# Performance work log

Hardware: AMD Instinct MI355X
Metric: run time of the kernel (lower is better)

Reference implementation:

```python
import jax, jax.numpy as jnp
import numpy as np

jax.config.update("jax_enable_x64", True)

P = 2038074743          # prime used by the ROBE-Z hash
BLOCK_K = 32            # tile sizes of the hashed reconstruction (kernel tile)
BLOCK_N = 32
INPUT_DIM = 8192
OUTPUT_DIM = 8192
HASH_SIZE = 1 << 22     # compressed parameter count
TOKENS = 512


def setup_inputs() -> dict:
    key = jax.random.key(0)
    k1, k2 = jax.random.split(key, 2)
    x = jax.random.normal(k1, (TOKENS, INPUT_DIM), dtype=jnp.float32)
    hashed_weight = jax.random.normal(k2, (HASH_SIZE,), dtype=jnp.float32) * 0.02
    bias = jnp.zeros((OUTPUT_DIM,), dtype=jnp.float32)
    # mirrors RzLinear._generate_random_numbers(seed): 4 random ints made even, prepended with P
    rng = np.random.RandomState(1024)
    r = rng.randint(0, P, size=(4,)).astype(np.int64)
    r = r + (r % 2)
    random_numbers = jnp.asarray(np.concatenate([np.array([P], dtype=np.int64), r]), dtype=jnp.int64)
    return {"x": x, "hashed_weight": hashed_weight, "bias": bias, "random_numbers": random_numbers}


def _weight_indices(random_numbers):
    """Hashed flat indices into hashed_weight for the dense [K, N] weight."""
    K, N = INPUT_DIM, OUTPUT_DIM
    kt, nt = K // BLOCK_K, N // BLOCK_N
    R1, R2, R3 = random_numbers[1], random_numbers[2], random_numbers[3]
    k_ids = jnp.arange(kt, dtype=jnp.int64)
    n_ids = jnp.arange(nt, dtype=jnp.int64)
    # per-tile start offset into the compressed array
    start = ((k_ids[:, None] * R3 + n_ids[None, :] * R2 + R1) % P) % (HASH_SIZE - BLOCK_K * BLOCK_N + 1)
    start = start.astype(jnp.int32)  # [kt, nt]
    off = (jnp.arange(BLOCK_K, dtype=jnp.int32)[:, None] * BLOCK_N
           + jnp.arange(BLOCK_N, dtype=jnp.int32)[None, :])  # [BK, BN], row-major within tile
    idx = start[:, None, :, None] + off[None, :, None, :]    # [kt, BK, nt, BN]
    return idx.reshape(K, N)


def reference(x, hashed_weight, bias, random_numbers):
    idx = _weight_indices(random_numbers)          # [K, N] int32
    W = hashed_weight[idx]                          # hashed-gather reconstruction, [K, N]
    out = jnp.matmul(x, W) + bias[None, :]          # [tokens, N]
    return out
```

## Files before the change

### kernel.cpp

```cpp
#include <hip/hip_runtime.h>
#include <hip/hip_fp16.h>

#define NDIM 8192
#define KDIM 8192
#define NT 256
#define MOD2 4193281
#define PRIME 2038074743LL

#define BM 128
#define BN 128
#define BK 32
#define KITER 64
#define ASTRIDE 40
#define BSLAB 1032

typedef _Float16 half8 __attribute__((ext_vector_type(8)));
typedef float floatx4 __attribute__((ext_vector_type(4)));

#define BARRIER() asm volatile("s_waitcnt lgkmcnt(0)\n\ts_barrier" ::: "memory")

__global__ __launch_bounds__(256) void prep_kernel(const float* __restrict__ x,
                                                   const float* __restrict__ hw,
                                                   const float* __restrict__ bias,
                                                   const int* __restrict__ rn,
                                                   __half* __restrict__ xh,
                                                   __half* __restrict__ hh,
                                                   int* __restrict__ starts,
                                                   float* __restrict__ out) {
    int b = blockIdx.x;
    int tid = threadIdx.x;
    if (b < 8192) {
        int i = b * 256 + tid;
        const float4* s; uint2* d; int j;
        if (i < (1 << 20)) { s = (const float4*)x;  d = (uint2*)xh; j = i; }
        else               { s = (const float4*)hw; d = (uint2*)hh; j = i - (1 << 20); }
        float4 v = s[j];
        __half2 h01 = __floats2half2_rn(v.x, v.y);
        __half2 h23 = __floats2half2_rn(v.z, v.w);
        uint2 w = {*(unsigned*)&h01, *(unsigned*)&h23};
        d[j] = w;
    } else if (b < 8192 + 4096) {
        int i = (b - 8192) * 256 + tid;
        float4 bv = *(const float4*)(bias + ((i & 2047) << 2));
        ((float4*)out)[i] = bv;
    } else {
        int t = (b - 12288) * 256 + tid;
        bool is64 = (rn[1] == 0 && rn[3] == 0);
        long long R1 = is64 ? rn[2] : rn[1];
        long long R2 = is64 ? rn[4] : rn[2];
        long long R3 = is64 ? rn[6] : rn[3];
        long long k_id = t >> 8, n_id = t & 255;
        long long v = (k_id * R3 + n_id * R2 + R1) % PRIME;
        starts[t] = (int)(v % MOD2);
    }
}

__global__ __launch_bounds__(256, 4) void gemm_kernel(
    const __half* __restrict__ xh, const __half* __restrict__ hh,
    const int* __restrict__ starts, float* __restrict__ out) {
    __shared__ __align__(16) __half As[2][BM * ASTRIDE];
    __shared__ __align__(16) __half Bs[2][4 * BSLAB];
    __shared__ int Ss[KITER * 4];

    const int tid = threadIdx.x;
    const int lane = tid & 63;
    const int wave = tid >> 6;
    const int wm = wave >> 1;
    const int wn = wave & 1;
    const int quad = lane >> 4;
    const int l16 = lane & 15;

    const int i = blockIdx.x;
    const int ks = i & 3;
    const int m_blk = (i >> 2) & 3;
    const int n_blk = i >> 4;
    const int gm0 = m_blk * BM;
    const int gn0 = n_blk * BN;
    const int kt0 = ks * KITER;
    const int n_id0 = n_blk * 4;

    Ss[tid] = starts[(kt0 + (tid >> 2)) * NT + n_id0 + (tid & 3)];

    const int a_row = tid >> 1;
    const int a_ch = tid & 1;
    const __half* aptr = xh + (size_t)(gm0 + a_row) * KDIM + kt0 * 32 + a_ch * 16;
    const unsigned a_woff = a_row * ASTRIDE + a_ch * 16;

    const int b_tile = tid >> 6;
    const int b_oct = (tid >> 4) & 3;
    const int b_np = tid & 15;
    const unsigned b_woff = b_oct * BSLAB + (b_tile * 32 + 2 * b_np) * 8;

    uint4 pa0, pa1;
    unsigned qE0, qE1, qE2, qE3, qE4, qE5, qE6, qE7;
    unsigned qO0, qO1, qO2, qO3, qO4, qO5, qO6, qO7;

#define LOADA(kp_) do {                                                        \
        pa0 = *(const uint4*)(aptr + (kp_) * 32);                              \
        pa1 = *(const uint4*)(aptr + (kp_) * 32 + 8);                          \
    } while (0)

#define LOADB(Q0, Q1, Q2, Q3, Q4, Q5, Q6, Q7, kp_) do {                        \
        int st = Ss[(kp_) * 4 + b_tile];                                       \
        const __half* src = hh + st + b_oct * 256 + b_np * 2;                  \
        Q0 = *(const unsigned*)(src);                                          \
        Q1 = *(const unsigned*)(src + 32);                                     \
        Q2 = *(const unsigned*)(src + 64);                                     \
        Q3 = *(const unsigned*)(src + 96);                                     \
        Q4 = *(const unsigned*)(src + 128);                                    \
        Q5 = *(const unsigned*)(src + 160);                                    \
        Q6 = *(const unsigned*)(src + 192);                                    \
        Q7 = *(const unsigned*)(src + 224);                                    \
    } while (0)

#define STORET(Q0, Q1, Q2, Q3, Q4, Q5, Q6, Q7, buf_) do {                      \
        *(uint4*)&As[buf_][a_woff] = pa0;                                      \
        *(uint4*)&As[buf_][a_woff + 8] = pa1;                                  \
        unsigned e0 = (Q0 & 0xffffu) | (Q1 << 16);                             \
        unsigned e1 = (Q2 & 0xffffu) | (Q3 << 16);                             \
        unsigned e2 = (Q4 & 0xffffu) | (Q5 << 16);                             \
        unsigned e3 = (Q6 & 0xffffu) | (Q7 << 16);                             \
        unsigned o0 = (Q0 >> 16) | (Q1 & 0xffff0000u);                         \
        unsigned o1 = (Q2 >> 16) | (Q3 & 0xffff0000u);                         \
        unsigned o2 = (Q4 >> 16) | (Q5 & 0xffff0000u);                         \
        unsigned o3 = (Q6 >> 16) | (Q7 & 0xffff0000u);                         \
        *(uint4*)&Bs[buf_][b_woff] = (uint4){e0, e1, e2, e3};                  \
        *(uint4*)&Bs[buf_][b_woff + 8] = (uint4){o0, o1, o2, o3};              \
    } while (0)

    floatx4 acc[4][4];
#pragma unroll
    for (int r = 0; r < 4; r++)
#pragma unroll
        for (int c = 0; c < 4; c++)
            acc[r][c] = (floatx4){0.f, 0.f, 0.f, 0.f};

#define FRAGS_MFMA(buf_) do {                                                  \
        half8 af[4], bf[4];                                                    \
        _Pragma("unroll")                                                      \
        for (int r = 0; r < 4; r++)                                            \
            af[r] = *(const half8*)&As[buf_][(wm * 64 + r * 16 + l16) * ASTRIDE + quad * 8]; \
        _Pragma("unroll")                                                      \
        for (int c = 0; c < 4; c++)                                            \
            bf[c] = *(const half8*)&Bs[buf_][quad * BSLAB + (wn * 64 + c * 16 + l16) * 8];   \
        _Pragma("unroll")                                                      \
        for (int r = 0; r < 4; r++)                                            \
            _Pragma("unroll")                                                  \
            for (int c = 0; c < 4; c++)                                        \
                acc[r][c] = __builtin_amdgcn_mfma_f32_16x16x32_f16(af[r], bf[c], acc[r][c], 0, 0, 0); \
    } while (0)

    BARRIER();
    LOADB(qE0, qE1, qE2, qE3, qE4, qE5, qE6, qE7, 0);
    LOADB(qO0, qO1, qO2, qO3, qO4, qO5, qO6, qO7, 1);
    LOADA(0);
    STORET(qE0, qE1, qE2, qE3, qE4, qE5, qE6, qE7, 0);
    BARRIER();

    for (int kp = 0; kp < KITER; kp += 2) {
        LOADA(kp + 1);
        if (kp + 2 < KITER)
            LOADB(qE0, qE1, qE2, qE3, qE4, qE5, qE6, qE7, kp + 2);
        FRAGS_MFMA(0);
        STORET(qO0, qO1, qO2, qO3, qO4, qO5, qO6, qO7, 1);
        BARRIER();

        if (kp + 2 < KITER) {
            LOADA(kp + 2);
            if (kp + 3 < KITER)
                LOADB(qO0, qO1, qO2, qO3, qO4, qO5, qO6, qO7, kp + 3);
        }
        FRAGS_MFMA(1);
        if (kp + 2 < KITER)
            STORET(qE0, qE1, qE2, qE3, qE4, qE5, qE6, qE7, 0);
        BARRIER();
    }

#pragma unroll
    for (int c = 0; c < 4; c++) {
        int col = gn0 + wn * 64 + c * 16 + l16;
#pragma unroll
        for (int r = 0; r < 4; r++) {
            int row0 = gm0 + wm * 64 + r * 16 + quad * 4;
#pragma unroll
            for (int e = 0; e < 4; e++)
                atomicAdd(&out[(size_t)(row0 + e) * NDIM + col], acc[r][c][e]);
        }
    }
#undef LOADA
#undef LOADB
#undef STORET
#undef FRAGS_MFMA
}

extern "C" void kernel_launch(void* const* d_in, const int* in_sizes, int n_in,
                              void* d_out, int out_size, void* d_ws, size_t ws_size,
                              hipStream_t stream) {
    const float* x = (const float*)d_in[0];
    const float* hw = (const float*)d_in[1];
    const float* bias = (const float*)d_in[2];
    const int* rn = (const int*)d_in[3];
    float* out = (float*)d_out;

    char* ws = (char*)d_ws;
    __half* xh = (__half*)ws;
    __half* hh = (__half*)(ws + (8u << 20));
    int* starts = (int*)(ws + (16u << 20));

    hipLaunchKernelGGL(prep_kernel, dim3(12544), dim3(256), 0, stream,
                       x, hw, bias, rn, xh, hh, starts, out);
    hipLaunchKernelGGL(gemm_kernel, dim3(1024), dim3(256), 0, stream, xh, hh, starts, out);
}
```

Measured before the change: 202.7 us.

## Fuse fp32-to-fp16 conversion into GEMM tile loads, drop prep conversion pass

Removes the separate prep pass that converted x and hashed_weight to fp16 in workspace. The GEMM now loads fp32 directly and converts to fp16 with packed round-toward-zero conversion while staging tiles into shared memory. This avoids a full read-and-write pass over 8M floats, but doubles global load bytes per tile inside the GEMM and adds register pressure for the wider staging buffers. Rounding also changes from round-to-nearest to truncation toward zero.

After: 392.1 us. 1.93x slower.

```diff
diff --git a/kernel.cpp b/kernel.cpp
--- a/kernel.cpp
+++ b/kernel.cpp
@@ -9,42 +9,35 @@
 
 #define BM 128
 #define BN 128
-#define BK 32
 #define KITER 64
 #define ASTRIDE 40
 #define BSLAB 1032
 
 typedef _Float16 half8 __attribute__((ext_vector_type(8)));
+typedef __fp16 fp16x2 __attribute__((ext_vector_type(2)));
 typedef float floatx4 __attribute__((ext_vector_type(4)));
 
 #define BARRIER() asm volatile("s_waitcnt lgkmcnt(0)\n\ts_barrier" ::: "memory")
 
-__global__ __launch_bounds__(256) void prep_kernel(const float* __restrict__ x,
-                                                   const float* __restrict__ hw,
-                                                   const float* __restrict__ bias,
+static __device__ __forceinline__ unsigned pkrtz(float a, float b) {
+    fp16x2 h = __builtin_amdgcn_cvt_pkrtz(a, b);
+    unsigned u;
+    __builtin_memcpy(&u, &h, 4);
+    return u;
+}
+
+__global__ __launch_bounds__(256) void prep_kernel(const float* __restrict__ bias,
                                                    const int* __restrict__ rn,
-                                                   __half* __restrict__ xh,
-                                                   __half* __restrict__ hh,
                                                    int* __restrict__ starts,
                                                    float* __restrict__ out) {
     int b = blockIdx.x;
     int tid = threadIdx.x;
-    if (b < 8192) {
+    if (b < 4096) {
         int i = b * 256 + tid;
-        const float4* s; uint2* d; int j;
-        if (i < (1 << 20)) { s = (const float4*)x;  d = (uint2*)xh; j = i; }
-        else               { s = (const float4*)hw; d = (uint2*)hh; j = i - (1 << 20); }
-        float4 v = s[j];
-        __half2 h01 = __floats2half2_rn(v.x, v.y);
-        __half2 h23 = __floats2half2_rn(v.z, v.w);
-        uint2 w = {*(unsigned*)&h01, *(unsigned*)&h23};
-        d[j] = w;
-    } else if (b < 8192 + 4096) {
-        int i = (b - 8192) * 256 + tid;
         float4 bv = *(const float4*)(bias + ((i & 2047) << 2));
         ((float4*)out)[i] = bv;
     } else {
-        int t = (b - 12288) * 256 + tid;
+        int t = (b - 4096) * 256 + tid;
         bool is64 = (rn[1] == 0 && rn[3] == 0);
         long long R1 = is64 ? rn[2] : rn[1];
         long long R2 = is64 ? rn[4] : rn[2];
@@ -56,7 +49,7 @@
 }
 
 __global__ __launch_bounds__(256, 4) void gemm_kernel(
-    const __half* __restrict__ xh, const __half* __restrict__ hh,
+    const float* __restrict__ x, const float* __restrict__ hw,
     const int* __restrict__ starts, float* __restrict__ out) {
     __shared__ __align__(16) __half As[2][BM * ASTRIDE];
     __shared__ __align__(16) __half Bs[2][4 * BSLAB];
@@ -83,7 +76,7 @@
 
     const int a_row = tid >> 1;
     const int a_ch = tid & 1;
-    const __half* aptr = xh + (size_t)(gm0 + a_row) * KDIM + kt0 * 32 + a_ch * 16;
+    const float* aptr = x + (size_t)(gm0 + a_row) * KDIM + kt0 * 32 + a_ch * 16;
     const unsigned a_woff = a_row * ASTRIDE + a_ch * 16;
 
     const int b_tile = tid >> 6;
@@ -91,41 +84,43 @@
     const int b_np = tid & 15;
     const unsigned b_woff = b_oct * BSLAB + (b_tile * 32 + 2 * b_np) * 8;
 
-    uint4 pa0, pa1;
-    unsigned qE0, qE1, qE2, qE3, qE4, qE5, qE6, qE7;
-    unsigned qO0, qO1, qO2, qO3, qO4, qO5, qO6, qO7;
+    float4 fa0, fa1, fa2, fa3;
+    float2 gE0, gE1, gE2, gE3, gE4, gE5, gE6, gE7;
+    float2 gO0, gO1, gO2, gO3, gO4, gO5, gO6, gO7;
 
 #define LOADA(kp_) do {                                                        \
-        pa0 = *(const uint4*)(aptr + (kp_) * 32);                              \
-        pa1 = *(const uint4*)(aptr + (kp_) * 32 + 8);                          \
-    } while (0)
-
-#define LOADB(Q0, Q1, Q2, Q3, Q4, Q5, Q6, Q7, kp_) do {                        \
+        fa0 = *(const float4*)(aptr + (kp_) * 32);                             \
+        fa1 = *(const float4*)(aptr + (kp_) * 32 + 4);                         \
+        fa2 = *(const float4*)(aptr + (kp_) * 32 + 8);                         \
+        fa3 = *(const float4*)(aptr + (kp_) * 32 + 12);                        \
+    } while (0)
+
+#define LOADB(G0, G1, G2, G3, G4, G5, G6, G7, kp_) do {                        \
         int st = Ss[(kp_) * 4 + b_tile];                                       \
-        const __half* src = hh + st + b_oct * 256 + b_np * 2;                  \
-        Q0 = *(const unsigned*)(src);                                          \
-        Q1 = *(const unsigned*)(src + 32);                                     \
-        Q2 = *(const unsigned*)(src + 64);                                     \
-        Q3 = *(const unsigned*)(src + 96);                                     \
-        Q4 = *(const unsigned*)(src + 128);                                    \
-        Q5 = *(const unsigned*)(src + 160);                                    \
-        Q6 = *(const unsigned*)(src + 192);                                    \
-        Q7 = *(const unsigned*)(src + 224);                                    \
-    } while (0)
-
-#define STORET(Q0, Q1, Q2, Q3, Q4, Q5, Q6, Q7, buf_) do {                      \
-        *(uint4*)&As[buf_][a_woff] = pa0;                                      \
-        *(uint4*)&As[buf_][a_woff + 8] = pa1;                                  \
-        unsigned e0 = (Q0 & 0xffffu) | (Q1 << 16);                             \
-        unsigned e1 = (Q2 & 0xffffu) | (Q3 << 16);                             \
-        unsigned e2 = (Q4 & 0xffffu) | (Q5 << 16);                             \
-        unsigned e3 = (Q6 & 0xffffu) | (Q7 << 16);                             \
-        unsigned o0 = (Q0 >> 16) | (Q1 & 0xffff0000u);                         \
-        unsigned o1 = (Q2 >> 16) | (Q3 & 0xffff0000u);                         \
-        unsigned o2 = (Q4 >> 16) | (Q5 & 0xffff0000u);                         \
-        unsigned o3 = (Q6 >> 16) | (Q7 & 0xffff0000u);                         \
-        *(uint4*)&Bs[buf_][b_woff] = (uint4){e0, e1, e2, e3};                  \
-        *(uint4*)&Bs[buf_][b_woff + 8] = (uint4){o0, o1, o2, o3};              \
+        const float* src = hw + st + b_oct * 256 + b_np * 2;                   \
+        G0 = *(const float2*)(src);                                            \
+        G1 = *(const float2*)(src + 32);                                       \
+        G2 = *(const float2*)(src + 64);                                       \
+        G3 = *(const float2*)(src + 96);                                       \
+        G4 = *(const float2*)(src + 128);                                      \
+        G5 = *(const float2*)(src + 160);                                      \
+        G6 = *(const float2*)(src + 192);                                      \
+        G7 = *(const float2*)(src + 224);                                      \
+    } while (0)
+
+#define STORET(G0, G1, G2, G3, G4, G5, G6, G7, buf_) do {                      \
+        uint4 wa0 = {pkrtz(fa0.x, fa0.y), pkrtz(fa0.z, fa0.w),                 \
+                     pkrtz(fa1.x, fa1.y), pkrtz(fa1.z, fa1.w)};                \
+        uint4 wa1 = {pkrtz(fa2.x, fa2.y), pkrtz(fa2.z, fa2.w),                 \
+                     pkrtz(fa3.x, fa3.y), pkrtz(fa3.z, fa3.w)};                \
+        *(uint4*)&As[buf_][a_woff] = wa0;                                      \
+        *(uint4*)&As[buf_][a_woff + 8] = wa1;                                  \
+        uint4 we = {pkrtz(G0.x, G1.x), pkrtz(G2.x, G3.x),                      \
+                    pkrtz(G4.x, G5.x), pkrtz(G6.x, G7.x)};                     \
+        uint4 wo = {pkrtz(G0.y, G1.y), pkrtz(G2.y, G3.y),                      \
+                    pkrtz(G4.y, G5.y), pkrtz(G6.y, G7.y)};                     \
+        *(uint4*)&Bs[buf_][b_woff] = we;                                       \
+        *(uint4*)&Bs[buf_][b_woff + 8] = wo;                                   \
     } while (0)
 
     floatx4 acc[4][4];
@@ -151,28 +146,28 @@
     } while (0)
 
     BARRIER();
-    LOADB(qE0, qE1, qE2, qE3, qE4, qE5, qE6, qE7, 0);
-    LOADB(qO0, qO1, qO2, qO3, qO4, qO5, qO6, qO7, 1);
+    LOADB(gE0, gE1, gE2, gE3, gE4, gE5, gE6, gE7, 0);
+    LOADB(gO0, gO1, gO2, gO3, gO4, gO5, gO6, gO7, 1);
     LOADA(0);
-    STORET(qE0, qE1, qE2, qE3, qE4, qE5, qE6, qE7, 0);
+    STORET(gE0, gE1, gE2, gE3, gE4, gE5, gE6, gE7, 0);
     BARRIER();
 
     for (int kp = 0; kp < KITER; kp += 2) {
         LOADA(kp + 1);
         if (kp + 2 < KITER)
-            LOADB(qE0, qE1, qE2, qE3, qE4, qE5, qE6, qE7, kp + 2);
+            LOADB(gE0, gE1, gE2, gE3, gE4, gE5, gE6, gE7, kp + 2);
         FRAGS_MFMA(0);
-        STORET(qO0, qO1, qO2, qO3, qO4, qO5, qO6, qO7, 1);
+        STORET(gO0, gO1, gO2, gO3, gO4, gO5, gO6, gO7, 1);
         BARRIER();
 
         if (kp + 2 < KITER) {
             LOADA(kp + 2);
             if (kp + 3 < KITER)
-                LOADB(qO0, qO1, qO2, qO3, qO4, qO5, qO6, qO7, kp + 3);
+                LOADB(gO0, gO1, gO2, gO3, gO4, gO5, gO6, gO7, kp + 3);
         }
         FRAGS_MFMA(1);
         if (kp + 2 < KITER)
-            STORET(qE0, qE1, qE2, qE3, qE4, qE5, qE6, qE7, 0);
+            STORET(gE0, gE1, gE2, gE3, gE4, gE5, gE6, gE7, 0);
         BARRIER();
     }
 
@@ -202,12 +197,9 @@
     const int* rn = (const int*)d_in[3];
     float* out = (float*)d_out;
 
-    char* ws = (char*)d_ws;
-    __half* xh = (__half*)ws;
-    __half* hh = (__half*)(ws + (8u << 20));
-    int* starts = (int*)(ws + (16u << 20));
-
-    hipLaunchKernelGGL(prep_kernel, dim3(12544), dim3(256), 0, stream,
-                       x, hw, bias, rn, xh, hh, starts, out);
-    hipLaunchKernelGGL(gemm_kernel, dim3(1024), dim3(256), 0, stream, xh, hh, starts, out);
-}
+    int* starts = (int*)d_ws;
+
+    hipLaunchKernelGGL(prep_kernel, dim3(4352), dim3(256), 0, stream,
+                       bias, rn, starts, out);
+    hipLaunchKernelGGL(gemm_kernel, dim3(1024), dim3(256), 0, stream, x, hw, starts, out);
+}
```
